# Performance work log

Measured on AMD Instinct MI355X. Metric: run time of the kernel, lower is better.

The kernel has to match this reference:

```python
import jax, jax.numpy as jnp
import numpy as np

B, N, C = 4, 4096, 256
NUM_HEADS = 8
NUM_GROUPS = 4  # num_groups2, recursive_index=True path
HEAD_DIM = C // NUM_HEADS
SCALE = HEAD_DIM ** -0.5


def setup_inputs() -> dict:
    key = jax.random.key(0)
    k_x, k_idx, k_qkv, k_proj, k_pb = jax.random.split(key, 5)
    x = jax.random.normal(k_x, (B, N, C), dtype=jnp.float32)
    idx = jax.random.permutation(k_idx, N)  # random token shuffle (torch.randperm)
    # nn.Linear params (torch convention: y = x @ W.T + b)
    w_qkv = jax.random.normal(k_qkv, (3 * C, C), dtype=jnp.float32) * (1.0 / np.sqrt(C))
    w_proj = jax.random.normal(k_proj, (C, C), dtype=jnp.float32) * (1.0 / np.sqrt(C))
    b_proj = jax.random.normal(k_pb, (C,), dtype=jnp.float32) * 0.01
    return {"x": x, "idx": idx, "w_qkv": w_qkv, "w_proj": w_proj, "b_proj": b_proj}


def reference(x, idx, w_qkv, w_proj, b_proj):
    g, H, d = NUM_GROUPS, NUM_HEADS, HEAD_DIM
    n = N // g  # tokens per group
    inverse = jnp.argsort(idx)
    xp = x[:, idx, :]  # shuffled tokens [B, N, C]
    # qkv projection then split into groups/heads: [B, g, n, 3, H, d]
    qkv = (xp @ w_qkv.T).reshape(B, g, n, 3, H, d)
    q = qkv[:, :, :, 0].transpose(0, 1, 3, 2, 4)  # [B, g, H, n, d]
    k = qkv[:, :, :, 1].transpose(0, 1, 3, 2, 4)
    v = qkv[:, :, :, 2].transpose(0, 1, 3, 2, 4)
    attn = jnp.einsum('bghnd,bghmd->bghnm', q, k) * SCALE  # [B, g, H, n, n]
    attn = jax.nn.softmax(attn, axis=-1)
    o = jnp.einsum('bghnm,bghmd->bghnd', attn, v)
    # [B, g, H, n, d] -> [B, g, n, H, d] -> [B, N, C] (group-major token order)
    o = o.transpose(0, 1, 3, 2, 4).reshape(B, N, C)
    o = o[:, inverse, :]  # undo the shuffle
    return o @ w_proj.T + b_proj
```

## Files before the change

kernel.cpp:

```cpp
#include <hip/hip_runtime.h>
#include <hip/hip_bf16.h>


typedef __attribute__((ext_vector_type(8))) short bf16x8;
typedef __attribute__((ext_vector_type(4))) float f32x4;

__device__ __forceinline__ unsigned short f2bf(float x){
  __hip_bfloat16 h = __float2bfloat16(x);
  return __builtin_bit_cast(unsigned short, h);
}

#define QSCALE (0.17677669529663687f * 1.4426950408889634f)


__global__ __launch_bounds__(256) void qkv_gemm(
    const float* __restrict__ x, const int* __restrict__ idx,
    const float* __restrict__ w_qkv,
    unsigned short* __restrict__ Qb, unsigned short* __restrict__ KF,
    unsigned short* __restrict__ VF)
{
  __shared__ unsigned short Alds[64*256];
  __shared__ unsigned short Blds[64*256];
  const int tid = threadIdx.x;
  const int m0 = blockIdx.x << 6;
  const int bb = m0 >> 12;
  const int gg = (m0 >> 10) & 3;
  const int j0 = m0 & 4095;

  #pragma unroll
  for (int it = 0; it < 8; ++it){
    int c = (it << 8) + tid;
    int row = c >> 5;
    int k8 = (c & 31) << 3;
    int srow = (bb << 12) + idx[j0 + row];
    const float4 f0 = *(const float4*)(x + srow*256 + k8);
    const float4 f1 = *(const float4*)(x + srow*256 + k8 + 4);
    bf16x8 v;
    v[0]=(short)f2bf(f0.x); v[1]=(short)f2bf(f0.y);
    v[2]=(short)f2bf(f0.z); v[3]=(short)f2bf(f0.w);
    v[4]=(short)f2bf(f1.x); v[5]=(short)f2bf(f1.y);
    v[6]=(short)f2bf(f1.z); v[7]=(short)f2bf(f1.w);
    int byt = ((row << 9) + (k8 << 1)) ^ ((row & 7) << 4);
    *(bf16x8*)((char*)Alds + byt) = v;
  }

  const int w  = tid >> 6, lane = tid & 63;
  const int lr = lane & 15, lg = lane >> 4;
  const int wr = w >> 1,  wc = w & 1;

  for (int nt = 0; nt < 6; ++nt){
    const int n0 = blockIdx.y * 384 + nt * 64;
    __syncthreads();
    #pragma unroll
    for (int it = 0; it < 8; ++it){
      int c = (it << 8) + tid;
      int row = c >> 5;
      int k8 = (c & 31) << 3;
      const float4 f0 = *(const float4*)(w_qkv + (n0+row)*256 + k8);
      const float4 f1 = *(const float4*)(w_qkv + (n0+row)*256 + k8 + 4);
      bf16x8 v;
      v[0]=(short)f2bf(f0.x); v[1]=(short)f2bf(f0.y);
      v[2]=(short)f2bf(f0.z); v[3]=(short)f2bf(f0.w);
      v[4]=(short)f2bf(f1.x); v[5]=(short)f2bf(f1.y);
      v[6]=(short)f2bf(f1.z); v[7]=(short)f2bf(f1.w);
      int byt = ((row << 9) + (k8 << 1)) ^ ((row & 7) << 4);
      *(bf16x8*)((char*)Blds + byt) = v;
    }
    __syncthreads();

    f32x4 acc[2][2];
    #pragma unroll
    for (int i=0;i<2;++i)
      #pragma unroll
      for (int j=0;j<2;++j)
        acc[i][j] = (f32x4){0.f,0.f,0.f,0.f};

    #pragma unroll
    for (int ks = 0; ks < 8; ++ks){
      bf16x8 af[2], bfr[2];
      int ka = (ks << 5) + (lg << 3);
      #pragma unroll
      for (int i=0;i<2;++i){
        int rowA = (wr << 5) + (i << 4) + lr;
        int bytA = ((rowA << 9) + (ka << 1)) ^ ((rowA & 7) << 4);
        af[i] = *(const bf16x8*)((const char*)Alds + bytA);
        int rowB = (wc << 5) + (i << 4) + lr;
        int bytB = ((rowB << 9) + (ka << 1)) ^ ((rowB & 7) << 4);
        bfr[i] = *(const bf16x8*)((const char*)Blds + bytB);
      }
      #pragma unroll
      for (int i=0;i<2;++i)
        #pragma unroll
        for (int j=0;j<2;++j)
          acc[i][j] = __builtin_amdgcn_mfma_f32_16x16x32_bf16(af[i], bfr[j], acc[i][j], 0, 0, 0);
    }

    #pragma unroll
    for (int i=0;i<2;++i){
      int mr0 = m0 + (wr << 5) + (i << 4) + (lg << 2);
      int nl0 = mr0 & 1023;
      int t   = nl0 >> 5;
      #pragma unroll
      for (int j=0;j<2;++j){
        int o = n0 + (wc << 5) + (j << 4) + lr;
        int s = o >> 8, h = (o >> 5) & 7, dd = o & 31;
        int head = ((bb << 2) + gg) * 8 + h;
        if (s == 2){
          int m = nl0 & 31;
          int lane2 = ((m >> 3) << 4) + (dd & 15);
          int half = dd >> 4;
          ushort4 pk;
          pk.x = f2bf(acc[i][j][0]); pk.y = f2bf(acc[i][j][1]);
          pk.z = f2bf(acc[i][j][2]); pk.w = f2bf(acc[i][j][3]);
          *(ushort4*)(VF + head*32768 + t*1024 + half*512 + lane2*8 + (m & 7)) = pk;
        } else if (s == 1){
          int r0 = nl0 & 31;
          int f  = (r0 >> 2) & 1;
          unsigned short* dst = KF + head*32768 + t*1024 + f*512
                               + ((((dd >> 3) << 4) + ((r0 >> 3) << 2)) << 3) + (dd & 7);
          dst[0]  = f2bf(acc[i][j][0]);
          dst[8]  = f2bf(acc[i][j][1]);
          dst[16] = f2bf(acc[i][j][2]);
          dst[24] = f2bf(acc[i][j][3]);
        } else {
          unsigned short* dst = Qb + head*32768 + dd;
          #pragma unroll
          for (int q=0;q<4;++q)
            dst[(nl0+q) << 5] = f2bf(acc[i][j][q] * QSCALE);
        }
      }
    }
  }
}

__device__ __forceinline__ void softmax16(
    const f32x4 s0, const f32x4 s1, const f32x4 s2, const f32x4 s3,
    bf16x8& pf0, bf16x8& pf1)
{
  float p0=__builtin_amdgcn_exp2f(s0[0]);  float p1=__builtin_amdgcn_exp2f(s0[1]);
  float p2=__builtin_amdgcn_exp2f(s0[2]);  float p3=__builtin_amdgcn_exp2f(s0[3]);
  float p4=__builtin_amdgcn_exp2f(s1[0]);  float p5=__builtin_amdgcn_exp2f(s1[1]);
  float p6=__builtin_amdgcn_exp2f(s1[2]);  float p7=__builtin_amdgcn_exp2f(s1[3]);
  float p8=__builtin_amdgcn_exp2f(s2[0]);  float p9=__builtin_amdgcn_exp2f(s2[1]);
  float p10=__builtin_amdgcn_exp2f(s2[2]); float p11=__builtin_amdgcn_exp2f(s2[3]);
  float p12=__builtin_amdgcn_exp2f(s3[0]); float p13=__builtin_amdgcn_exp2f(s3[1]);
  float p14=__builtin_amdgcn_exp2f(s3[2]); float p15=__builtin_amdgcn_exp2f(s3[3]);

  pf0[0]=(short)f2bf(p0);  pf0[1]=(short)f2bf(p1);
  pf0[2]=(short)f2bf(p2);  pf0[3]=(short)f2bf(p3);
  pf0[4]=(short)f2bf(p4);  pf0[5]=(short)f2bf(p5);
  pf0[6]=(short)f2bf(p6);  pf0[7]=(short)f2bf(p7);
  pf1[0]=(short)f2bf(p8);  pf1[1]=(short)f2bf(p9);
  pf1[2]=(short)f2bf(p10); pf1[3]=(short)f2bf(p11);
  pf1[4]=(short)f2bf(p12); pf1[5]=(short)f2bf(p13);
  pf1[6]=(short)f2bf(p14); pf1[7]=(short)f2bf(p15);
}

__global__ __launch_bounds__(256, 4) void attn_kernel(
    const unsigned short* __restrict__ Qb, const unsigned short* __restrict__ KF,
    const unsigned short* __restrict__ VF, unsigned short* __restrict__ OB)
{
  __shared__ __align__(16) char lds[32768];
  const int tid  = threadIdx.x;
  const int head = blockIdx.x >> 3;
  const int qblk = blockIdx.x & 7;
  const int lane = tid & 63;
  const int w  = tid >> 6;
  const int lr = lane & 15, lg = lane >> 4;
  const int q0 = qblk * 128 + w * 32;

  const unsigned short* kf = KF + head*32768;
  const unsigned short* vf = VF + head*32768;
  const unsigned short* qbase = Qb + head*32768;

  {
    bf16x8 k0 = *(const bf16x8*)(kf + tid*8);
    bf16x8 k1 = *(const bf16x8*)(kf + 2048 + tid*8);
    bf16x8 v0 = *(const bf16x8*)(vf + tid*8);
    bf16x8 v1 = *(const bf16x8*)(vf + 2048 + tid*8);
    *(bf16x8*)(lds + tid*16)          = k0;
    *(bf16x8*)(lds + 4096 + tid*16)   = k1;
    *(bf16x8*)(lds + 8192 + tid*16)   = v0;
    *(bf16x8*)(lds + 12288 + tid*16)  = v1;
  }
  bf16x8 qfA = *(const bf16x8*)(qbase + (q0 + lr)*32 + (lg << 3));
  bf16x8 qfB = *(const bf16x8*)(qbase + (q0 + 16 + lr)*32 + (lg << 3));

  const short one_bf = (short)0x3F80;
  bf16x8 onesf = {one_bf,one_bf,one_bf,one_bf,one_bf,one_bf,one_bf,one_bf};

  f32x4 o0A={0.f,0.f,0.f,0.f}, o1A={0.f,0.f,0.f,0.f};
  f32x4 o0B={0.f,0.f,0.f,0.f}, o1B={0.f,0.f,0.f,0.f};
  f32x4 lsA={0.f,0.f,0.f,0.f}, lsB={0.f,0.f,0.f,0.f};
  const f32x4 zz={0.f,0.f,0.f,0.f};

  __syncthreads();
  int cur = 0;
  for (int it = 0; it < 8; ++it){
    bf16x8 kr0, kr1, vr0, vr1;
    const bool pf = (it < 7);
    if (pf){
      const unsigned short* kg = kf + (it+1)*4096 + tid*8;
      const unsigned short* vg = vf + (it+1)*4096 + tid*8;
      kr0 = *(const bf16x8*)(kg);
      kr1 = *(const bf16x8*)(kg + 2048);
      vr0 = *(const bf16x8*)(vg);
      vr1 = *(const bf16x8*)(vg + 2048);
    }

    const char* KL = lds + cur*16384 + lane*16;
    const char* VL = KL + 8192;
    #pragma unroll
    for (int hh = 0; hh < 2; ++hh){
      const char* kp_ = KL + hh*4096;
      const char* vp_ = VL + hh*4096;
      bf16x8 kA0 = *(const bf16x8*)(kp_);
      bf16x8 kB0 = *(const bf16x8*)(kp_ + 1024);
      bf16x8 kA1 = *(const bf16x8*)(kp_ + 2048);
      bf16x8 kB1 = *(const bf16x8*)(kp_ + 3072);
      bf16x8 v00 = *(const bf16x8*)(vp_);
      bf16x8 v01 = *(const bf16x8*)(vp_ + 1024);
      bf16x8 v10 = *(const bf16x8*)(vp_ + 2048);
      bf16x8 v11 = *(const bf16x8*)(vp_ + 3072);

      __builtin_amdgcn_s_setprio(1);
      f32x4 sA0A = __builtin_amdgcn_mfma_f32_16x16x32_bf16(kA0, qfA, zz, 0, 0, 0);
      f32x4 sB0A = __builtin_amdgcn_mfma_f32_16x16x32_bf16(kB0, qfA, zz, 0, 0, 0);
      f32x4 sA1A = __builtin_amdgcn_mfma_f32_16x16x32_bf16(kA1, qfA, zz, 0, 0, 0);
      f32x4 sB1A = __builtin_amdgcn_mfma_f32_16x16x32_bf16(kB1, qfA, zz, 0, 0, 0);
      f32x4 sA0B = __builtin_amdgcn_mfma_f32_16x16x32_bf16(kA0, qfB, zz, 0, 0, 0);
      f32x4 sB0B = __builtin_amdgcn_mfma_f32_16x16x32_bf16(kB0, qfB, zz, 0, 0, 0);
      f32x4 sA1B = __builtin_amdgcn_mfma_f32_16x16x32_bf16(kA1, qfB, zz, 0, 0, 0);
      f32x4 sB1B = __builtin_amdgcn_mfma_f32_16x16x32_bf16(kB1, qfB, zz, 0, 0, 0);
      __builtin_amdgcn_s_setprio(0);

      bf16x8 pf0A, pf1A, pf0B, pf1B;
      softmax16(sA0A, sB0A, sA1A, sB1A, pf0A, pf1A);
      __builtin_amdgcn_s_setprio(1);
      o0A = __builtin_amdgcn_mfma_f32_16x16x32_bf16(pf0A, v00, o0A, 0, 0, 0);
      o1A = __builtin_amdgcn_mfma_f32_16x16x32_bf16(pf0A, v01, o1A, 0, 0, 0);
      o0A = __builtin_amdgcn_mfma_f32_16x16x32_bf16(pf1A, v10, o0A, 0, 0, 0);
      o1A = __builtin_amdgcn_mfma_f32_16x16x32_bf16(pf1A, v11, o1A, 0, 0, 0);
      lsA = __builtin_amdgcn_mfma_f32_16x16x32_bf16(pf0A, onesf, lsA, 0, 0, 0);
      lsA = __builtin_amdgcn_mfma_f32_16x16x32_bf16(pf1A, onesf, lsA, 0, 0, 0);
      __builtin_amdgcn_s_setprio(0);
      softmax16(sA0B, sB0B, sA1B, sB1B, pf0B, pf1B);
      __builtin_amdgcn_s_setprio(1);
      o0B = __builtin_amdgcn_mfma_f32_16x16x32_bf16(pf0B, v00, o0B, 0, 0, 0);
      o1B = __builtin_amdgcn_mfma_f32_16x16x32_bf16(pf0B, v01, o1B, 0, 0, 0);
      o0B = __builtin_amdgcn_mfma_f32_16x16x32_bf16(pf1B, v10, o0B, 0, 0, 0);
      o1B = __builtin_amdgcn_mfma_f32_16x16x32_bf16(pf1B, v11, o1B, 0, 0, 0);
      lsB = __builtin_amdgcn_mfma_f32_16x16x32_bf16(pf0B, onesf, lsB, 0, 0, 0);
      lsB = __builtin_amdgcn_mfma_f32_16x16x32_bf16(pf1B, onesf, lsB, 0, 0, 0);
      __builtin_amdgcn_s_setprio(0);
    }

    if (pf){
      char* db = lds + (cur^1)*16384;
      *(bf16x8*)(db + tid*16)          = kr0;
      *(bf16x8*)(db + 4096 + tid*16)   = kr1;
      *(bf16x8*)(db + 8192 + tid*16)   = vr0;
      *(bf16x8*)(db + 12288 + tid*16)  = vr1;
    }
    __syncthreads();
    cur ^= 1;
  }

  const int bI = head >> 5, gI = (head >> 3) & 3, hI = head & 7;
  unsigned short* obase = OB + (bI*4096 + gI*1024 + q0)*256 + hI*32;
  #pragma unroll
  for (int q = 0; q < 4; ++q){
    float iA = 1.0f / lsA[q];
    obase[((lg << 2) + q)*256 + lr]      = f2bf(o0A[q] * iA);
    obase[((lg << 2) + q)*256 + 16 + lr] = f2bf(o1A[q] * iA);
    float iB = 1.0f / lsB[q];
    obase[(16 + (lg << 2) + q)*256 + lr]      = f2bf(o0B[q] * iB);
    obase[(16 + (lg << 2) + q)*256 + 16 + lr] = f2bf(o1B[q] * iB);
  }
}

__global__ __launch_bounds__(256) void proj_gemm(
    const unsigned short* __restrict__ OB, const float* __restrict__ w_proj,
    const float* __restrict__ b_proj, const int* __restrict__ idx,
    float* __restrict__ out)
{
  __shared__ unsigned short Alds[64*256];
  __shared__ unsigned short Blds[64*256];
  const int tid = threadIdx.x;
  const int m0 = blockIdx.x << 6;
  const int bb = m0 >> 12;

  #pragma unroll
  for (int it = 0; it < 8; ++it){
    int c = (it << 8) + tid;
    int row = c >> 5;
    int k8 = (c & 31) << 3;
    int byt = ((row << 9) + (k8 << 1)) ^ ((row & 7) << 4);
    *(bf16x8*)((char*)Alds + byt) = *(const bf16x8*)(OB + (m0+row)*256 + k8);
  }

  const int w  = tid >> 6, lane = tid & 63;
  const int lr = lane & 15, lg = lane >> 4;
  const int wr = w >> 1,  wc = w & 1;

  for (int nt = 0; nt < 2; ++nt){
    const int n0 = blockIdx.y * 128 + nt * 64;
    __syncthreads();
    #pragma unroll
    for (int it = 0; it < 8; ++it){
      int c = (it << 8) + tid;
      int row = c >> 5;
      int k8 = (c & 31) << 3;
      const float4 f0 = *(const float4*)(w_proj + (n0+row)*256 + k8);
      const float4 f1 = *(const float4*)(w_proj + (n0+row)*256 + k8 + 4);
      bf16x8 v;
      v[0]=(short)f2bf(f0.x); v[1]=(short)f2bf(f0.y);
      v[2]=(short)f2bf(f0.z); v[3]=(short)f2bf(f0.w);
      v[4]=(short)f2bf(f1.x); v[5]=(short)f2bf(f1.y);
      v[6]=(short)f2bf(f1.z); v[7]=(short)f2bf(f1.w);
      int byt = ((row << 9) + (k8 << 1)) ^ ((row & 7) << 4);
      *(bf16x8*)((char*)Blds + byt) = v;
    }
    __syncthreads();

    f32x4 acc[2][2];
    #pragma unroll
    for (int i=0;i<2;++i)
      #pragma unroll
      for (int j=0;j<2;++j)
        acc[i][j] = (f32x4){0.f,0.f,0.f,0.f};

    #pragma unroll
    for (int ks = 0; ks < 8; ++ks){
      bf16x8 af[2], bfr[2];
      int ka = (ks << 5) + (lg << 3);
      #pragma unroll
      for (int i=0;i<2;++i){
        int rowA = (wr << 5) + (i << 4) + lr;
        int bytA = ((rowA << 9) + (ka << 1)) ^ ((rowA & 7) << 4);
        af[i] = *(const bf16x8*)((const char*)Alds + bytA);
        int rowB = (wc << 5) + (i << 4) + lr;
        int bytB = ((rowB << 9) + (ka << 1)) ^ ((rowB & 7) << 4);
        bfr[i] = *(const bf16x8*)((const char*)Blds + bytB);
      }
      #pragma unroll
      for (int i=0;i<2;++i)
        #pragma unroll
        for (int j=0;j<2;++j)
          acc[i][j] = __builtin_amdgcn_mfma_f32_16x16x32_bf16(af[i], bfr[j], acc[i][j], 0, 0, 0);
    }

    #pragma unroll
    for (int i=0;i<2;++i){
      int mr0 = m0 + (wr << 5) + (i << 4) + (lg << 2);
      int rd[4];
      #pragma unroll
      for (int q=0;q<4;++q)
        rd[q] = (bb << 12) + idx[(mr0 + q) & 4095];
      #pragma unroll
      for (int j=0;j<2;++j){
        int o = n0 + (wc << 5) + (j << 4) + lr;
        float bias = b_proj[o];
        #pragma unroll
        for (int q=0;q<4;++q)
          out[rd[q]*256 + o] = acc[i][j][q] + bias;
      }
    }
  }
}

extern "C" void kernel_launch(void* const* d_in, const int* in_sizes, int n_in,
                              void* d_out, int out_size, void* d_ws, size_t ws_size,
                              hipStream_t stream)
{
  const float* x      = (const float*)d_in[0];
  const int*   idx    = (const int*)  d_in[1];
  const float* w_qkv  = (const float*)d_in[2];
  const float* w_proj = (const float*)d_in[3];
  const float* b_proj = (const float*)d_in[4];
  float* out = (float*)d_out;

  char* ws = (char*)d_ws;
  unsigned short* Qb = (unsigned short*)(ws);
  unsigned short* KF = (unsigned short*)(ws + (8u  << 20));
  unsigned short* VF = (unsigned short*)(ws + (16u << 20));
  unsigned short* OB = (unsigned short*)(ws + (24u << 20));

  qkv_gemm<<<dim3(256, 2), 256, 0, stream>>>(x, idx, w_qkv, Qb, KF, VF);
  attn_kernel<<<dim3(1024), 256, 0, stream>>>(Qb, KF, VF, OB);
  proj_gemm<<<dim3(256, 2), 256, 0, stream>>>(OB, w_proj, b_proj, idx, out);
}
```

Baseline: 61.98 us.

## Retile QKV GEMM to 128x128 tiles with K-sliced register-prefetched pipeline

The QKV projection GEMM now uses 128x128 output tiles instead of 64x64 tiles computed six times per block. It also loops over K in 32-wide slices, staging only 128x32 A and B slices in shared memory. The next slice's fp32 global loads are issued into registers before the current slice's MFMAs, which overlaps memory latency with compute and cuts LDS use so more blocks can be resident. The grid changes from 256x2 to 128x6. Each wave now holds 16 accumulators, which raises register pressure, and the kernel adds extra barriers per K step.

```diff
diff --git a/kernel.cpp b/kernel.cpp
--- a/kernel.cpp
+++ b/kernel.cpp
@@ -10,124 +10,143 @@
   return __builtin_bit_cast(unsigned short, h);
 }
 
+__device__ __forceinline__ bf16x8 cvt8(const float4 f0, const float4 f1){
+  bf16x8 v;
+  v[0]=(short)f2bf(f0.x); v[1]=(short)f2bf(f0.y);
+  v[2]=(short)f2bf(f0.z); v[3]=(short)f2bf(f0.w);
+  v[4]=(short)f2bf(f1.x); v[5]=(short)f2bf(f1.y);
+  v[6]=(short)f2bf(f1.z); v[7]=(short)f2bf(f1.w);
+  return v;
+}
+
 #define QSCALE (0.17677669529663687f * 1.4426950408889634f)
 
 
-__global__ __launch_bounds__(256) void qkv_gemm(
+__global__ __launch_bounds__(256, 3) void qkv_gemm(
     const float* __restrict__ x, const int* __restrict__ idx,
     const float* __restrict__ w_qkv,
     unsigned short* __restrict__ Qb, unsigned short* __restrict__ KF,
     unsigned short* __restrict__ VF)
 {
-  __shared__ unsigned short Alds[64*256];
-  __shared__ unsigned short Blds[64*256];
+  __shared__ __align__(16) unsigned short Asl[128*64];
+  __shared__ __align__(16) unsigned short Bsl[128*64];
   const int tid = threadIdx.x;
-  const int m0 = blockIdx.x << 6;
-  const int bb = m0 >> 12;
-  const int gg = (m0 >> 10) & 3;
-  const int j0 = m0 & 4095;
-
-  #pragma unroll
-  for (int it = 0; it < 8; ++it){
+  const int bx = blockIdx.x, by = blockIdx.y;
+  const int m0 = bx << 7;
+  const int bb = bx >> 5;
+  const int gg = (bx >> 3) & 3;
+  const int j0 = (bx & 31) << 7;
+  const int n0 = by << 7;
+
+  int srow[2], brow[2], wb[2];
+  #pragma unroll
+  for (int it = 0; it < 2; ++it){
     int c = (it << 8) + tid;
-    int row = c >> 5;
-    int k8 = (c & 31) << 3;
-    int srow = (bb << 12) + idx[j0 + row];
-    const float4 f0 = *(const float4*)(x + srow*256 + k8);
-    const float4 f1 = *(const float4*)(x + srow*256 + k8 + 4);
-    bf16x8 v;
-    v[0]=(short)f2bf(f0.x); v[1]=(short)f2bf(f0.y);
-    v[2]=(short)f2bf(f0.z); v[3]=(short)f2bf(f0.w);
-    v[4]=(short)f2bf(f1.x); v[5]=(short)f2bf(f1.y);
-    v[6]=(short)f2bf(f1.z); v[7]=(short)f2bf(f1.w);
-    int byt = ((row << 9) + (k8 << 1)) ^ ((row & 7) << 4);
-    *(bf16x8*)((char*)Alds + byt) = v;
-  }
-
-  const int w  = tid >> 6, lane = tid & 63;
+    int row = c >> 2;
+    int k8 = (c & 3) << 3;
+    srow[it] = (bb << 12) + idx[j0 + row];
+    brow[it] = n0 + row;
+    wb[it] = ((row << 7) + (k8 << 1)) ^ ((row & 7) << 4);
+  }
+
+  #pragma unroll
+  for (int it = 0; it < 2; ++it){
+    int k8 = (((it << 8) + tid) & 3) << 3;
+    const float* xs = x + srow[it]*256 + k8;
+    const float* wsp = w_qkv + brow[it]*256 + k8;
+    *(bf16x8*)((char*)Asl + wb[it]) = cvt8(*(const float4*)(xs), *(const float4*)(xs+4));
+    *(bf16x8*)((char*)Bsl + wb[it]) = cvt8(*(const float4*)(wsp), *(const float4*)(wsp+4));
+  }
+  __syncthreads();
+
+  const int lane = tid & 63;
+  const int w = tid >> 6, wr = w >> 1, wc = w & 1;
   const int lr = lane & 15, lg = lane >> 4;
-  const int wr = w >> 1,  wc = w & 1;
-
-  for (int nt = 0; nt < 6; ++nt){
-    const int n0 = blockIdx.y * 384 + nt * 64;
+  const int ka = lg << 3;
+
+  f32x4 acc[4][4];
+  #pragma unroll
+  for (int il = 0; il < 4; ++il)
+    #pragma unroll
+    for (int jl = 0; jl < 4; ++jl)
+      acc[il][jl] = (f32x4){0.f,0.f,0.f,0.f};
+
+  for (int st = 0; st < 8; ++st){
+    float4 a0[2], a1[2], c0[2], c1[2];
+    const bool pf = (st < 7);
+    if (pf){
+      int kb = (st + 1) << 5;
+      #pragma unroll
+      for (int it = 0; it < 2; ++it){
+        int k8 = (((it << 8) + tid) & 3) << 3;
+        const float* xs = x + srow[it]*256 + kb + k8;
+        const float* wsp = w_qkv + brow[it]*256 + kb + k8;
+        a0[it] = *(const float4*)(xs);  a1[it] = *(const float4*)(xs + 4);
+        c0[it] = *(const float4*)(wsp); c1[it] = *(const float4*)(wsp + 4);
+      }
+    }
+
+    bf16x8 af[4], bfr[4];
+    #pragma unroll
+    for (int il = 0; il < 4; ++il){
+      int rowA = (wr << 6) + (il << 4) + lr;
+      af[il] = *(const bf16x8*)((const char*)Asl + (((rowA << 7) + (ka << 1)) ^ ((rowA & 7) << 4)));
+      int rowB = (wc << 6) + (il << 4) + lr;
+      bfr[il] = *(const bf16x8*)((const char*)Bsl + (((rowB << 7) + (ka << 1)) ^ ((rowB & 7) << 4)));
+    }
+    __builtin_amdgcn_s_setprio(1);
+    #pragma unroll
+    for (int il = 0; il < 4; ++il)
+      #pragma unroll
+      for (int jl = 0; jl < 4; ++jl)
+        acc[il][jl] = __builtin_amdgcn_mfma_f32_16x16x32_bf16(af[il], bfr[jl], acc[il][jl], 0, 0, 0);
+    __builtin_amdgcn_s_setprio(0);
+
     __syncthreads();
-    #pragma unroll
-    for (int it = 0; it < 8; ++it){
-      int c = (it << 8) + tid;
-      int row = c >> 5;
-      int k8 = (c & 31) << 3;
-      const float4 f0 = *(const float4*)(w_qkv + (n0+row)*256 + k8);
-      const float4 f1 = *(const float4*)(w_qkv + (n0+row)*256 + k8 + 4);
-      bf16x8 v;
-      v[0]=(short)f2bf(f0.x); v[1]=(short)f2bf(f0.y);
-      v[2]=(short)f2bf(f0.z); v[3]=(short)f2bf(f0.w);
-      v[4]=(short)f2bf(f1.x); v[5]=(short)f2bf(f1.y);
-      v[6]=(short)f2bf(f1.z); v[7]=(short)f2bf(f1.w);
-      int byt = ((row << 9) + (k8 << 1)) ^ ((row & 7) << 4);
-      *(bf16x8*)((char*)Blds + byt) = v;
-    }
-    __syncthreads();
-
-    f32x4 acc[2][2];
-    #pragma unroll
-    for (int i=0;i<2;++i)
-      #pragma unroll
-      for (int j=0;j<2;++j)
-        acc[i][j] = (f32x4){0.f,0.f,0.f,0.f};
-
-    #pragma unroll
-    for (int ks = 0; ks < 8; ++ks){
-      bf16x8 af[2], bfr[2];
-      int ka = (ks << 5) + (lg << 3);
-      #pragma unroll
-      for (int i=0;i<2;++i){
-        int rowA = (wr << 5) + (i << 4) + lr;
-        int bytA = ((rowA << 9) + (ka << 1)) ^ ((rowA & 7) << 4);
-        af[i] = *(const bf16x8*)((const char*)Alds + bytA);
-        int rowB = (wc << 5) + (i << 4) + lr;
-        int bytB = ((rowB << 9) + (ka << 1)) ^ ((rowB & 7) << 4);
-        bfr[i] = *(const bf16x8*)((const char*)Blds + bytB);
+    if (pf){
+      #pragma unroll
+      for (int it = 0; it < 2; ++it){
+        *(bf16x8*)((char*)Asl + wb[it]) = cvt8(a0[it], a1[it]);
+        *(bf16x8*)((char*)Bsl + wb[it]) = cvt8(c0[it], c1[it]);
       }
-      #pragma unroll
-      for (int i=0;i<2;++i)
+      __syncthreads();
+    }
+  }
+
+  const int s = by >> 1;
+  const int hbase = ((bb << 2) + gg) << 3;
+  #pragma unroll
+  for (int il = 0; il < 4; ++il){
+    int mr0 = m0 + (wr << 6) + (il << 4) + (lg << 2);
+    int nl0 = mr0 & 1023;
+    int t   = nl0 >> 5;
+    #pragma unroll
+    for (int jl = 0; jl < 4; ++jl){
+      int ocol = ((by & 1) << 7) + (wc << 6) + (jl << 4) + lr;
+      int h  = ocol >> 5, dd = ocol & 31;
+      int head = hbase + h;
+      if (s == 2){
+        int m = nl0 & 31;
+        int lane2 = ((m >> 3) << 4) + (dd & 15);
+        int half = dd >> 4;
+        ushort4 pk;
+        pk.x = f2bf(acc[il][jl][0]); pk.y = f2bf(acc[il][jl][1]);
+        pk.z = f2bf(acc[il][jl][2]); pk.w = f2bf(acc[il][jl][3]);
+        *(ushort4*)(VF + head*32768 + t*1024 + half*512 + lane2*8 + (m & 7)) = pk;
+      } else if (s == 1){
+        int r0 = nl0 & 31;
+        int f  = (r0 >> 2) & 1;
+        unsigned short* dst = KF + head*32768 + t*1024 + f*512
+                             + ((((dd >> 3) << 4) + ((r0 >> 3) << 2)) << 3) + (dd & 7);
+        dst[0]  = f2bf(acc[il][jl][0]);
+        dst[8]  = f2bf(acc[il][jl][1]);
+        dst[16] = f2bf(acc[il][jl][2]);
+        dst[24] = f2bf(acc[il][jl][3]);
+      } else {
+        unsigned short* dst = Qb + head*32768 + dd;
         #pragma unroll
-        for (int j=0;j<2;++j)
-          acc[i][j] = __builtin_amdgcn_mfma_f32_16x16x32_bf16(af[i], bfr[j], acc[i][j], 0, 0, 0);
-    }
-
-    #pragma unroll
-    for (int i=0;i<2;++i){
-      int mr0 = m0 + (wr << 5) + (i << 4) + (lg << 2);
-      int nl0 = mr0 & 1023;
-      int t   = nl0 >> 5;
-      #pragma unroll
-      for (int j=0;j<2;++j){
-        int o = n0 + (wc << 5) + (j << 4) + lr;
-        int s = o >> 8, h = (o >> 5) & 7, dd = o & 31;
-        int head = ((bb << 2) + gg) * 8 + h;
-        if (s == 2){
-          int m = nl0 & 31;
-          int lane2 = ((m >> 3) << 4) + (dd & 15);
-          int half = dd >> 4;
-          ushort4 pk;
-          pk.x = f2bf(acc[i][j][0]); pk.y = f2bf(acc[i][j][1]);
-          pk.z = f2bf(acc[i][j][2]); pk.w = f2bf(acc[i][j][3]);
-          *(ushort4*)(VF + head*32768 + t*1024 + half*512 + lane2*8 + (m & 7)) = pk;
-        } else if (s == 1){
-          int r0 = nl0 & 31;
-          int f  = (r0 >> 2) & 1;
-          unsigned short* dst = KF + head*32768 + t*1024 + f*512
-                               + ((((dd >> 3) << 4) + ((r0 >> 3) << 2)) << 3) + (dd & 7);
-          dst[0]  = f2bf(acc[i][j][0]);
-          dst[8]  = f2bf(acc[i][j][1]);
-          dst[16] = f2bf(acc[i][j][2]);
-          dst[24] = f2bf(acc[i][j][3]);
-        } else {
-          unsigned short* dst = Qb + head*32768 + dd;
-          #pragma unroll
-          for (int q=0;q<4;++q)
-            dst[(nl0+q) << 5] = f2bf(acc[i][j][q] * QSCALE);
-        }
+        for (int q = 0; q < 4; ++q)
+          dst[(nl0 + q) << 5] = f2bf(acc[il][jl][q] * QSCALE);
       }
     }
   }
@@ -386,7 +405,7 @@
   unsigned short* VF = (unsigned short*)(ws + (16u << 20));
   unsigned short* OB = (unsigned short*)(ws + (24u << 20));
 
-  qkv_gemm<<<dim3(256, 2), 256, 0, stream>>>(x, idx, w_qkv, Qb, KF, VF);
+  qkv_gemm<<<dim3(128, 6), 256, 0, stream>>>(x, idx, w_qkv, Qb, KF, VF);
   attn_kernel<<<dim3(1024), 256, 0, stream>>>(Qb, KF, VF, OB);
   proj_gemm<<<dim3(256, 2), 256, 0, stream>>>(OB, w_proj, b_proj, idx, out);
 }
```

After: 60.99 us. About the same (-1.6%).
